# Optimization experiments

Hardware: AMD Instinct MI355X
Metric: run time of the kernel (lower is better)

The kernel has to match this reference:

```python
import jax, jax.numpy as jnp
import numpy as np

N, D, B, P, T = 2048, 64, 64, 16384, 262144
EPS = 1e-6        # const.eps in the original repo
LAST_TIME = 1.0   # init_time = 0


def setup_inputs() -> dict:
    key = jax.random.key(0)
    k = jax.random.split(key, 8)
    x0 = jax.random.normal(k[0], (N, D), dtype=jnp.float32)
    v = 0.1 * jax.random.normal(k[1], (B, N, D), dtype=jnp.float32)
    beta = jax.random.normal(k[2], (N,), dtype=jnp.float32)
    bins_rwidth = jax.random.normal(k[3], (B,), dtype=jnp.float32)
    # distinct node pairs (i != j) to avoid degenerate zero-distance pairs
    i = jax.random.randint(k[4], (P,), 0, N, dtype=jnp.int32)
    off = jax.random.randint(k[5], (P,), 1, N, dtype=jnp.int32)
    node_pairs = jnp.stack([i, (i + off) % N], axis=0)  # [2, P]
    event_times = jax.random.uniform(k[6], (T,), dtype=jnp.float32) * LAST_TIME
    event_pair_idx = jax.random.randint(k[7], (T,), 0, P, dtype=jnp.int32)
    return {"x0": x0, "v": v, "beta": beta, "bins_rwidth": bins_rwidth,
            "event_times": event_times, "node_pairs": node_pairs,
            "event_pair_idx": event_pair_idx}


def reference(x0, v, beta, bins_rwidth, event_times, node_pairs, event_pair_idx):
    # bin bounds: softmax(relative widths) -> cumsum over the timeline
    bounds = jnp.concatenate([jnp.zeros((1,), x0.dtype),
                              jnp.cumsum(jax.nn.softmax(bins_rwidth)) * LAST_TIME])  # [B+1]
    widths = bounds[1:] - bounds[:-1]          # [B]
    inner = bounds[1:-1]                       # bucketize boundaries

    i, j = node_pairs[0], node_pairs[1]
    dx0 = x0[i] - x0[j]                        # [P, D]
    dv = v[:, i, :] - v[:, j, :]               # [B, P, D]
    # cumulative displacement at each bin boundary
    cum = jnp.concatenate([jnp.zeros((1, dx0.shape[0], dx0.shape[1]), dx0.dtype),
                           jnp.cumsum(dv * widths[:, None, None], axis=0)], axis=0)  # [B+1, P, D]
    beta_sum = beta[i] + beta[j]               # [P]

    # ---- intensity integral over the bin bounds (closed form per bin) ----
    idx_b = jnp.searchsorted(inner, bounds, side='right')          # torch.bucketize right=True
    rem_b = bounds - bounds[idx_b]
    xt_b = dx0[None] + cum[idx_b] + dv[idx_b] * rem_b[:, None, None]  # [B+1, P, D]
    norm_b = jnp.linalg.norm(xt_b, axis=2)                         # [B+1, P]
    numer = norm_b * jnp.exp(beta_sum[None, :] - norm_b)
    dot1 = jnp.sum(xt_b[1:] * dv, axis=2)                          # [B, P]
    dot0 = jnp.sum(xt_b[:-1] * dv, axis=2)
    integral = jnp.sum(numer[1:] / (dot1 + EPS) - numer[:-1] / (dot0 + EPS))

    # ---- ragged event log-intensities (flattened: events -> pair ids) ----
    idx_e = jnp.searchsorted(inner, event_times, side='right')     # [T]
    rem_e = event_times - bounds[idx_e]
    pid = event_pair_idx
    xt_e = dx0[pid] + cum[idx_e, pid] + dv[idx_e, pid] * rem_e[:, None]  # [T, D]
    dist_e = jnp.linalg.norm(xt_e, axis=1)
    non_integral = jnp.sum(beta_sum[pid] - dist_e)

    # NLL = -(-integral + non_integral)
    return integral - non_integral
```

## Files before the change

### kernel.cpp

```cpp
#include <hip/hip_runtime.h>

#define NN 2048
#define DD 64
#define BB 64
#define PP 16384
#define TT 262144
#define EPSF 1e-6f
#define SS ((size_t)NN * DD)


typedef unsigned uv2 __attribute__((ext_vector_type(2)));
using bf16x8 = __attribute__((ext_vector_type(8))) short;
using f32x4v = __attribute__((ext_vector_type(4))) float;

template <int CTRL, int RM = 0xF, bool BC = true>
__device__ __forceinline__ float dpp_add(float x) {
    int y = __builtin_amdgcn_update_dpp(0, __float_as_int(x), CTRL, RM, 0xF, BC);
    return x + __int_as_float(y);
}

template <int PAT>
__device__ __forceinline__ float swz_add(float x) {
    return x + __int_as_float(__builtin_amdgcn_ds_swizzle(__float_as_int(x), PAT));
}

__device__ __forceinline__ float xor16_add(float x) {
#if __has_builtin(__builtin_amdgcn_permlane16_swap)
    uv2 r = __builtin_amdgcn_permlane16_swap(__float_as_uint(x), __float_as_uint(x),
                                             false, false);
    return __uint_as_float(r.x) + __uint_as_float(r.y);
#else
    return swz_add<0x401F>(x);
#endif
}
__device__ __forceinline__ float xor32_add(float x) {
#if __has_builtin(__builtin_amdgcn_permlane32_swap)
    uv2 r = __builtin_amdgcn_permlane32_swap(__float_as_uint(x), __float_as_uint(x),
                                             false, false);
    return __uint_as_float(r.x) + __uint_as_float(r.y);
#else
    return x + __shfl_xor(x, 32, 64);
#endif
}

__device__ __forceinline__ float reduce1(float a) {
    a = dpp_add<0xB1>(a);
    a = dpp_add<0x4E>(a);
    a = dpp_add<0x141>(a);
    a = swz_add<0x201F>(a);
    a = xor16_add(a);
    a = xor32_add(a);
    return a;
}

__device__ __forceinline__ float incl_scan(float x) {
    x = dpp_add<0x111>(x);
    x = dpp_add<0x112>(x);
    x = dpp_add<0x114>(x);
    x = dpp_add<0x118>(x);
    x = dpp_add<0x142, 0xA, false>(x);
    x = dpp_add<0x143, 0xC, false>(x);
    return x;
}

__device__ __forceinline__ unsigned short f2bf(float f) {
    unsigned u = __float_as_uint(f);
    unsigned r = (u + 0x7FFFu + ((u >> 16) & 1u)) >> 16;
    return (unsigned short)r;
}
__device__ __forceinline__ float bf_lo(unsigned u) { return __uint_as_float(u << 16); }
__device__ __forceinline__ float bf_hi(unsigned u) { return __uint_as_float(u & 0xFFFF0000u); }

__device__ __forceinline__ unsigned cvt_pk_bf(float lo, float hi) {
    unsigned r;
    asm("v_cvt_pk_bf16_f32 %0, %1, %2" : "=v"(r) : "v"(lo), "v"(hi));
    return r;
}
__device__ __forceinline__ float bpermf(float v, int srclane) {
    return __int_as_float(__builtin_amdgcn_ds_bpermute(srclane << 2, __float_as_int(v)));
}

__global__ void k_bounds(const float* __restrict__ brw, float* __restrict__ bounds,
                         float* __restrict__ widths, float* __restrict__ innerPad,
                         int* __restrict__ cnt, double* __restrict__ acc) {
    if (blockIdx.x != 0) {
        int t = (blockIdx.x - 1) * 64 + threadIdx.x;
#pragma unroll
        for (int k = 0; k < 4; k++) cnt[t * 4 + k] = 0;
        if (blockIdx.x == 1 && threadIdx.x == 0) acc[0] = 0.0;
        return;
    }
    int lane = threadIdx.x;
    float w = brw[lane];
    float m = w;
#pragma unroll
    for (int s = 32; s >= 1; s >>= 1) m = fmaxf(m, __shfl_xor(m, s, 64));
    float e = expf(w - m);
    float tot = e;
#pragma unroll
    for (int s = 32; s >= 1; s >>= 1) tot += __shfl_xor(tot, s, 64);
    float sm = e / tot;
    float c = sm;
#pragma unroll
    for (int off = 1; off < 64; off <<= 1) {
        float t = __shfl_up(c, off, 64);
        if (lane >= off) c += t;
    }
    float cexcl = __shfl_up(c, 1, 64);
    if (lane == 0) cexcl = 0.f;
    if (lane == 0) bounds[0] = 0.f;
    bounds[lane + 1] = c;
    widths[lane] = c - cexcl;
    innerPad[lane] = (lane == 63) ? 3.4e38f : c;
}

__global__ __launch_bounds__(256) void k_convert_hist(const float* __restrict__ v,
                                                      unsigned* __restrict__ vh32,
                                                      const int* __restrict__ pairs,
                                                      int* __restrict__ cnt) {
    if (blockIdx.x >= NN / 4) {
        int t = (blockIdx.x - NN / 4) * 256 + threadIdx.x;
        atomicAdd(&cnt[pairs[t]], 1);
        return;
    }
    int wid = threadIdx.x >> 6, lane = threadIdx.x & 63;
    int n = blockIdx.x * 4 + wid;
    int sub = lane >> 5;
    int dp = (lane & 31) * 2;
    unsigned* __restrict__ dst = vh32 + ((size_t)n * BB * DD) / 2;
#pragma unroll
    for (int c = 0; c < 32; c++) {
        int b = c * 2 + sub;
        float2 f = *(const float2*)(v + (size_t)b * SS + (size_t)n * DD + dp);
        unsigned pk = (unsigned)f2bf(f.x) | ((unsigned)f2bf(f.y) << 16);
        dst[(b * DD + dp) / 2] = pk;
    }
}

__global__ __launch_bounds__(1024) void k_scan2(const int* __restrict__ cnt,
                                                int* __restrict__ cursor) {
    __shared__ int waveTot[16];
    __shared__ int waveOff[16];
    int tid = threadIdx.x;
    int a = cnt[tid * 2], b = cnt[tid * 2 + 1];
    int s = a + b;
    int lane = tid & 63, wid = tid >> 6;
    int incl = s;
#pragma unroll
    for (int off = 1; off < 64; off <<= 1) {
        int t2 = __shfl_up(incl, off, 64);
        if (lane >= off) incl += t2;
    }
    if (lane == 63) waveTot[wid] = incl;
    __syncthreads();
    if (tid == 0) {
        int r = 0;
        for (int w = 0; w < 16; w++) { waveOff[w] = r; r += waveTot[w]; }
    }
    __syncthreads();
    int run = waveOff[wid] + (incl - s);
    cursor[tid * 2] = run;
    cursor[tid * 2 + 1] = run + a;
}

__global__ void k_scatter2(const int* __restrict__ pairs, int* __restrict__ cursor,
                           int* __restrict__ perm) {
    int t = blockIdx.x * 256 + threadIdx.x;
    int pos = atomicAdd(&cursor[pairs[t]], 1);
    perm[pos] = t;
}

__global__ __launch_bounds__(256, 2) void k_pairs(
    const float* __restrict__ x0, const uint4* __restrict__ vh4,
    const float* __restrict__ beta, const int* __restrict__ pairs,
    const int* __restrict__ perm, const float* __restrict__ widths,
    float4* __restrict__ table, double* __restrict__ acc_out) {
    __shared__ double bacc[4];
    const int wid = threadIdx.x >> 6;
    const int lane = threadIdx.x & 63;
    const int bid = blockIdx.x;
    const int vb = ((bid & 7) << 6) | (bid >> 3);
    const int pbase = (vb * 4 + wid) * 8;

    int pk[8], ik[8], jk[8];
    float bs[8];
#pragma unroll
    for (int k = 0; k < 8; k++) pk[k] = perm[pbase + k];
#pragma unroll
    for (int k = 0; k < 8; k++) {
        ik[k] = pairs[pk[k]];
        jk[k] = pairs[PP + pk[k]];
    }
#pragma unroll
    for (int k = 0; k < 8; k++) bs[k] = beta[ik[k]] + beta[jk[k]];

    float wv[4][4];
#pragma unroll
    for (int tm = 0; tm < 4; tm++)
#pragma unroll
        for (int r = 0; r < 4; r++)
            wv[tm][r] = widths[16 * tm + (lane >> 4) * 4 + r];
    const float wl = widths[lane];
    const int laneterm = (lane & 15) * 8 + (lane >> 4);
    const int nl = lane & 15;
    const int mb = (lane >> 4) * 4;

    uint4 ra0[8], rb0[8], ra1[8], rb1[8];
    float xi0, xj0, xi1, xj1;

#define ISSUE(RA, RB, XI, XJ, k_)                                            \
    {                                                                        \
        const uint4* Vi = vh4 + (size_t)ik[k_] * 512 + laneterm;             \
        const uint4* Vj = vh4 + (size_t)jk[k_] * 512 + laneterm;             \
        _Pragma("unroll") for (int t = 0; t < 4; t++) {                      \
            RA[t * 2 + 0] = Vi[t * 128];                                     \
            RA[t * 2 + 1] = Vi[t * 128 + 4];                                 \
            RB[t * 2 + 0] = Vj[t * 128];                                     \
            RB[t * 2 + 1] = Vj[t * 128 + 4];                                 \
        }                                                                    \
        XI = x0[ik[k_] * DD + lane];                                         \
        XJ = x0[jk[k_] * DD + lane];                                         \
    }

    double accd = 0.0;

#define STEP(RA, RB, XI, XJ, k_, NEXTISSUE)                                                    \
    {                                                                                          \
        const float bsum = bs[k_];                                                             \
        float dx0 = XI - XJ;                                                                   \
        float n2_0 = reduce1(dx0 * dx0);                                                       \
        float rr0 = __builtin_amdgcn_sqrtf(n2_0);                                              \
        float numer0 = rr0 * __expf(bsum - rr0);                                               \
        bf16x8 F[8];                                                                           \
        _Pragma("unroll") for (int f = 0; f < 8; f++) {                                        \
            uint4 q;                                                                           \
            q.x = cvt_pk_bf(bf_lo(RA[f].x) - bf_lo(RB[f].x), bf_hi(RA[f].x) - bf_hi(RB[f].x)); \
            q.y = cvt_pk_bf(bf_lo(RA[f].y) - bf_lo(RB[f].y), bf_hi(RA[f].y) - bf_hi(RB[f].y)); \
            q.z = cvt_pk_bf(bf_lo(RA[f].z) - bf_lo(RB[f].z), bf_hi(RA[f].z) - bf_hi(RB[f].z)); \
            q.w = cvt_pk_bf(bf_lo(RA[f].w) - bf_lo(RB[f].w), bf_hi(RA[f].w) - bf_hi(RB[f].w)); \
            union { uint4 u; bf16x8 s; } cv;                                                   \
            cv.u = q;                                                                          \
            F[f] = cv.s;                                                                       \
        }                                                                                      \
        NEXTISSUE                                                                              \
        bf16x8 AX[2];                                                                          \
        _Pragma("unroll") for (int kb = 0; kb < 2; kb++) {                                     \
            unsigned u[4];                                                                     \
            _Pragma("unroll") for (int c2 = 0; c2 < 4; c2++) {                                 \
                int k0 = kb * 32 + ((lane >> 4) << 3) + c2 * 2;                                \
                u[c2] = cvt_pk_bf(bpermf(dx0, k0), bpermf(dx0, k0 + 1));                       \
            }                                                                                  \
            uint4 q;                                                                           \
            bool z = (lane & 15) != 0;                                                         \
            q.x = z ? 0u : u[0]; q.y = z ? 0u : u[1];                                          \
            q.z = z ? 0u : u[2]; q.w = z ? 0u : u[3];                                          \
            union { uint4 uu; bf16x8 s; } cv;                                                  \
            cv.uu = q;                                                                         \
            AX[kb] = cv.s;                                                                     \
        }                                                                                      \
        f32x4v g00 = {0.f, 0.f, 0.f, 0.f}, g01 = g00, g02 = g00, g03 = g00;                    \
        f32x4v g11 = g00, g12 = g00, g13 = g00, g22 = g00, g23 = g00, g33 = g00;               \
        GMM(g00, 0, 0) GMM(g01, 0, 1) GMM(g02, 0, 2) GMM(g03, 0, 3)                            \
        GMM(g11, 1, 1) GMM(g12, 1, 2) GMM(g13, 1, 3)                                           \
        GMM(g22, 2, 2) GMM(g23, 2, 3) GMM(g33, 3, 3)                                           \
        float c00, c01, c02, c03;                                                              \
        {                                                                                      \
            f32x4v ca = {0.f, 0.f, 0.f, 0.f};                                                  \
            CMM(0) c00 = ca[0]; ca = {0.f, 0.f, 0.f, 0.f};                                     \
            CMM(1) c01 = ca[0]; ca = {0.f, 0.f, 0.f, 0.f};                                     \
            CMM(2) c02 = ca[0]; ca = {0.f, 0.f, 0.f, 0.f};                                     \
            CMM(3) c03 = ca[0];                                                                \
        }                                                                                      \
        float c0v;                                                                             \
        {                                                                                      \
            float b0 = bpermf(c00, lane & 15);                                                 \
            float b1 = bpermf(c01, lane & 15);                                                 \
            float b2 = bpermf(c02, lane & 15);                                                 \
            float b3 = bpermf(c03, lane & 15);                                                 \
            int g = lane >> 4;                                                                 \
            c0v = (g == 0) ? b0 : (g == 1) ? b1 : (g == 2) ? b2 : b3;                          \
        }                                                                                      \
        float Sv = 0.f, qv = 0.f;                                                              \
        { float sp = 0.f, qp = 0.f;                                 DIAG(g00, 0) FINTN(0) }    \
        { float sp = OFFT(g01, 0), qp = 0.f;                        DIAG(g11, 1) FINTN(1) }    \
        { float sp = OFFT(g02, 0) + OFFT(g12, 1), qp = 0.f;         DIAG(g22, 2) FINTN(2) }    \
        { float sp = OFFT(g03, 0) + OFFT(g13, 1) + OFFT(g23, 2), qp = 0.f;                     \
                                                                    DIAG(g33, 3) FINTN(3) }    \
        float d0r = c0v + Sv;                                                                  \
        float qqr = qv;                                                                        \
        float tt = wl * fmaf(wl, qqr, 2.f * d0r);                                              \
        float incl = incl_scan(tt);                                                            \
        float n2L = fmaxf(n2_0 + (incl - tt), 0.f);                                            \
        float n2R = fmaxf(n2_0 + incl, 0.f);                                                   \
        float rrR = __builtin_amdgcn_sqrtf(n2R);                                               \
        float numerR = rrR * __expf(bsum - rrR);                                               \
        float numerL = __int_as_float(                                                         \
            __builtin_amdgcn_update_dpp(0, __float_as_int(numerR), 0x138, 0xF, 0xF, true));    \
        numerL = (lane == 0) ? numer0 : numerL;                                                \
        float pd = fmaf(wl, qqr, d0r);                                                         \
        float term = numerR * __builtin_amdgcn_rcpf(pd + EPSF)                                 \
                   - numerL * __builtin_amdgcn_rcpf(d0r + EPSF);                               \
        float acc = reduce1(term);                                                             \
        table[(size_t)pk[k_] * BB + lane] = make_float4(n2L, d0r, qqr, bsum);                  \
        accd += (double)acc;                                                                   \
    }

#define GMM(acc, ta, tb)                                                                       \
    acc = __builtin_amdgcn_mfma_f32_16x16x32_bf16(F[(ta)*2 + 0], F[(tb)*2 + 0], acc, 0, 0, 0); \
    acc = __builtin_amdgcn_mfma_f32_16x16x32_bf16(F[(ta)*2 + 1], F[(tb)*2 + 1], acc, 0, 0, 0);
#define CMM(tb)                                                                       \
    ca = __builtin_amdgcn_mfma_f32_16x16x32_bf16(AX[0], F[(tb)*2 + 0], ca, 0, 0, 0); \
    ca = __builtin_amdgcn_mfma_f32_16x16x32_bf16(AX[1], F[(tb)*2 + 1], ca, 0, 0, 0);
#define OFFT(gt, t_) (wv[t_][0] * gt[0] + wv[t_][1] * gt[1] + wv[t_][2] * gt[2] + wv[t_][3] * gt[3])
#define DIAG(d, t_)                                       \
    sp += (mb + 0 < nl) ? wv[t_][0] * d[0] : 0.f;         \
    sp += (mb + 1 < nl) ? wv[t_][1] * d[1] : 0.f;         \
    sp += (mb + 2 < nl) ? wv[t_][2] * d[2] : 0.f;         \
    sp += (mb + 3 < nl) ? wv[t_][3] * d[3] : 0.f;         \
    qp += (mb + 0 == nl) ? d[0] : 0.f;                    \
    qp += (mb + 1 == nl) ? d[1] : 0.f;                    \
    qp += (mb + 2 == nl) ? d[2] : 0.f;                    \
    qp += (mb + 3 == nl) ? d[3] : 0.f;
#define FINTN(t_)                                         \
    sp = xor16_add(sp); sp = xor32_add(sp);               \
    qp = xor16_add(qp); qp = xor32_add(qp);               \
    if ((lane >> 4) == t_) { Sv = sp; qv = qp; }

    ISSUE(ra0, rb0, xi0, xj0, 0)
    ISSUE(ra1, rb1, xi1, xj1, 1)

    STEP(ra0, rb0, xi0, xj0, 0, ISSUE(ra0, rb0, xi0, xj0, 2))
    STEP(ra1, rb1, xi1, xj1, 1, ISSUE(ra1, rb1, xi1, xj1, 3))
    STEP(ra0, rb0, xi0, xj0, 2, ISSUE(ra0, rb0, xi0, xj0, 4))
    STEP(ra1, rb1, xi1, xj1, 3, ISSUE(ra1, rb1, xi1, xj1, 5))
    STEP(ra0, rb0, xi0, xj0, 4, ISSUE(ra0, rb0, xi0, xj0, 6))
    STEP(ra1, rb1, xi1, xj1, 5, ISSUE(ra1, rb1, xi1, xj1, 7))
    STEP(ra0, rb0, xi0, xj0, 6, )
    STEP(ra1, rb1, xi1, xj1, 7, )

#undef ISSUE
#undef STEP
#undef GMM
#undef CMM
#undef OFFT
#undef DIAG
#undef FINTN

    if (lane == 0) bacc[wid] = accd;
    __syncthreads();
    if (threadIdx.x == 0)
        atomicAdd(acc_out, bacc[0] + bacc[1] + bacc[2] + bacc[3]);
}

__global__ __launch_bounds__(256) void k_events(
    const float* __restrict__ times, const int* __restrict__ epid,
    const float* __restrict__ bounds, const float* __restrict__ innerPad,
    const float4* __restrict__ table, double* __restrict__ acc_out) {
    __shared__ float si[64];
    __shared__ float sb[BB + 1];
    __shared__ double wacc[4];
    int tid = threadIdx.x;
    if (tid < 64) si[tid] = innerPad[tid];
    if (tid <= BB) sb[tid] = bounds[tid];
    __syncthreads();
    int g = (blockIdx.x * 256 + tid) * 2;
    float2 tm2 = *(const float2*)(times + g);
    int2 pd2 = *(const int2*)(epid + g);
    float tms[2] = {tm2.x, tm2.y};
    int pids[2] = {pd2.x, pd2.y};
    int cc[2];
    float rem[2];
#pragma unroll
    for (int k = 0; k < 2; k++) {
        int c = 0;
        float tm = tms[k];
#pragma unroll
        for (int s = 32; s >= 1; s >>= 1)
            if (si[c + s - 1] <= tm) c += s;
        cc[k] = c;
        rem[k] = tm - sb[c];
    }
    float4 e0 = table[(size_t)pids[0] * BB + cc[0]];
    float4 e1 = table[(size_t)pids[1] * BB + cc[1]];
    float eacc;
    {
        float d2 = fmaxf(fmaf(rem[0], fmaf(rem[0], e0.z, 2.f * e0.y), e0.x), 0.f);
        eacc = e0.w - __builtin_amdgcn_sqrtf(d2);
        d2 = fmaxf(fmaf(rem[1], fmaf(rem[1], e1.z, 2.f * e1.y), e1.x), 0.f);
        eacc += e1.w - __builtin_amdgcn_sqrtf(d2);
    }
    float val = reduce1(eacc);
    if ((tid & 63) == 0) wacc[tid >> 6] = (double)val;
    __syncthreads();
    if (tid == 0)
        atomicAdd(acc_out, -(wacc[0] + wacc[1] + wacc[2] + wacc[3]));
}

__global__ void k_finalize(const double* __restrict__ acc, float* __restrict__ out) {
    out[0] = (float)(*acc);
}

extern "C" void kernel_launch(void* const* d_in, const int* in_sizes, int n_in,
                              void* d_out, int out_size, void* d_ws, size_t ws_size,
                              hipStream_t stream) {
    const float* x0     = (const float*)d_in[0];
    const float* v      = (const float*)d_in[1];
    const float* beta   = (const float*)d_in[2];
    const float* brw    = (const float*)d_in[3];
    const float* etimes = (const float*)d_in[4];
    const int*   pairs  = (const int*)d_in[5];
    const int*   epid   = (const int*)d_in[6];

    char* ws = (char*)d_ws;
    double* acc     = (double*)ws;
    int* cnt        = (int*)(ws + 1024);
    int* cursor     = (int*)(ws + 9216);
    int* perm       = (int*)(ws + 17408);
    float* bounds   = (float*)(ws + 82944);
    float* widths   = (float*)(ws + 83456);
    float* innerPad = (float*)(ws + 83968);
    float4* table   = (float4*)(ws + 84480);
    unsigned* vh32  = (unsigned*)(ws + 84480 + (size_t)PP * BB * 16);

    hipLaunchKernelGGL(k_bounds, dim3(9), dim3(64), 0, stream, brw, bounds, widths,
                       innerPad, cnt, acc);
    hipLaunchKernelGGL(k_convert_hist, dim3(NN / 4 + PP / 256), dim3(256), 0, stream,
                       v, vh32, pairs, cnt);
    hipLaunchKernelGGL(k_scan2, dim3(1), dim3(1024), 0, stream, cnt, cursor);
    hipLaunchKernelGGL(k_scatter2, dim3(PP / 256), dim3(256), 0, stream, pairs, cursor, perm);
    hipLaunchKernelGGL(k_pairs, dim3(PP / 32), dim3(256), 0, stream, x0, (const uint4*)vh32,
                       beta, pairs, perm, widths, table, acc);
    hipLaunchKernelGGL(k_events, dim3(TT / 512), dim3(256), 0, stream, etimes, epid,
                       bounds, innerPad, table, acc);
    hipLaunchKernelGGL(k_finalize, dim3(1), dim3(1), 0, stream, acc, (float*)d_out);
}
```

Measured before the change: 76.86 us.

## Fuse preprocessing kernels into one launch and finalize via last-block counter

Merges bounds computation, the v-to-bf16 conversion, the pair histogram, the scan and the scatter into a single kernel, k_pre. The histogram, scan and permutation now run in one block using shared-memory atomics. The conversion and the table writes use nontemporal vector loads and stores, and the MFMA section is raised with s_setprio. The separate finalize kernel is replaced by a last-block-done counter in k_events. Together these remove four launches and the global-memory round trips for counts and cursors, at the cost of serialising all the permutation work in one block.

```diff
diff --git a/kernel.cpp b/kernel.cpp
--- a/kernel.cpp
+++ b/kernel.cpp
@@ -10,6 +10,8 @@
 
 
 typedef unsigned uv2 __attribute__((ext_vector_type(2)));
+typedef float fx4 __attribute__((ext_vector_type(4)));
+typedef unsigned ux4 __attribute__((ext_vector_type(4)));
 using bf16x8 = __attribute__((ext_vector_type(8))) short;
 using f32x4v = __attribute__((ext_vector_type(4))) float;
 
@@ -63,10 +65,9 @@
     return x;
 }
 
-__device__ __forceinline__ unsigned short f2bf(float f) {
+__device__ __forceinline__ unsigned f2bf(float f) {
     unsigned u = __float_as_uint(f);
-    unsigned r = (u + 0x7FFFu + ((u >> 16) & 1u)) >> 16;
-    return (unsigned short)r;
+    return (u + 0x7FFFu + ((u >> 16) & 1u)) >> 16;
 }
 __device__ __forceinline__ float bf_lo(unsigned u) { return __uint_as_float(u << 16); }
 __device__ __forceinline__ float bf_hi(unsigned u) { return __uint_as_float(u & 0xFFFF0000u); }
@@ -80,70 +81,73 @@
     return __int_as_float(__builtin_amdgcn_ds_bpermute(srclane << 2, __float_as_int(v)));
 }
 
-__global__ void k_bounds(const float* __restrict__ brw, float* __restrict__ bounds,
-                         float* __restrict__ widths, float* __restrict__ innerPad,
-                         int* __restrict__ cnt, double* __restrict__ acc) {
-    if (blockIdx.x != 0) {
-        int t = (blockIdx.x - 1) * 64 + threadIdx.x;
-#pragma unroll
-        for (int k = 0; k < 4; k++) cnt[t * 4 + k] = 0;
-        if (blockIdx.x == 1 && threadIdx.x == 0) acc[0] = 0.0;
-        return;
-    }
-    int lane = threadIdx.x;
-    float w = brw[lane];
-    float m = w;
-#pragma unroll
-    for (int s = 32; s >= 1; s >>= 1) m = fmaxf(m, __shfl_xor(m, s, 64));
-    float e = expf(w - m);
-    float tot = e;
-#pragma unroll
-    for (int s = 32; s >= 1; s >>= 1) tot += __shfl_xor(tot, s, 64);
-    float sm = e / tot;
-    float c = sm;
-#pragma unroll
-    for (int off = 1; off < 64; off <<= 1) {
-        float t = __shfl_up(c, off, 64);
-        if (lane >= off) c += t;
-    }
-    float cexcl = __shfl_up(c, 1, 64);
-    if (lane == 0) cexcl = 0.f;
-    if (lane == 0) bounds[0] = 0.f;
-    bounds[lane + 1] = c;
-    widths[lane] = c - cexcl;
-    innerPad[lane] = (lane == 63) ? 3.4e38f : c;
-}
-
-__global__ __launch_bounds__(256) void k_convert_hist(const float* __restrict__ v,
-                                                      unsigned* __restrict__ vh32,
-                                                      const int* __restrict__ pairs,
-                                                      int* __restrict__ cnt) {
-    if (blockIdx.x >= NN / 4) {
-        int t = (blockIdx.x - NN / 4) * 256 + threadIdx.x;
-        atomicAdd(&cnt[pairs[t]], 1);
-        return;
-    }
-    int wid = threadIdx.x >> 6, lane = threadIdx.x & 63;
-    int n = blockIdx.x * 4 + wid;
-    int sub = lane >> 5;
-    int dp = (lane & 31) * 2;
-    unsigned* __restrict__ dst = vh32 + ((size_t)n * BB * DD) / 2;
-#pragma unroll
-    for (int c = 0; c < 32; c++) {
-        int b = c * 2 + sub;
-        float2 f = *(const float2*)(v + (size_t)b * SS + (size_t)n * DD + dp);
-        unsigned pk = (unsigned)f2bf(f.x) | ((unsigned)f2bf(f.y) << 16);
-        dst[(b * DD + dp) / 2] = pk;
-    }
-}
-
-__global__ __launch_bounds__(1024) void k_scan2(const int* __restrict__ cnt,
-                                                int* __restrict__ cursor) {
+__global__ __launch_bounds__(1024) void k_pre(
+    const float* __restrict__ v, unsigned* __restrict__ vh32,
+    const float* __restrict__ brw, float* __restrict__ bounds,
+    float* __restrict__ widths, float* __restrict__ innerPad,
+    const int* __restrict__ pairs, int* __restrict__ perm,
+    double* __restrict__ acc, int* __restrict__ done) {
+    __shared__ int scnt[2048];
     __shared__ int waveTot[16];
     __shared__ int waveOff[16];
-    int tid = threadIdx.x;
-    int a = cnt[tid * 2], b = cnt[tid * 2 + 1];
-    int s = a + b;
+    const int bid = blockIdx.x;
+    const int tid = threadIdx.x;
+
+    if (bid < 1024) {
+        const int bin = bid >> 4;
+        const int node0 = (bid & 15) << 7;
+        const fx4* __restrict__ src =
+            (const fx4*)(v + (size_t)bin * SS + (size_t)node0 * DD);
+        fx4 f0 = __builtin_nontemporal_load(src + tid * 2);
+        fx4 f1 = __builtin_nontemporal_load(src + tid * 2 + 1);
+        const int nn = tid >> 3;
+        const int d = (tid & 7) * 8;
+        ux4 o;
+        o.x = f2bf(f0.x) | (f2bf(f0.y) << 16);
+        o.y = f2bf(f0.z) | (f2bf(f0.w) << 16);
+        o.z = f2bf(f1.x) | (f2bf(f1.y) << 16);
+        o.w = f2bf(f1.z) | (f2bf(f1.w) << 16);
+        *(ux4*)(vh32 + (size_t)(node0 + nn) * 2048 + bin * 32 + d / 2) = o;
+        return;
+    }
+
+    if (bid == 1024) {
+        if (tid == 64) *acc = 0.0;
+        if (tid == 65) *done = 0;
+        if (tid >= 64) return;
+        int lane = tid;
+        float w = brw[lane];
+        float m = w;
+#pragma unroll
+        for (int s = 32; s >= 1; s >>= 1) m = fmaxf(m, __shfl_xor(m, s, 64));
+        float e = expf(w - m);
+        float tot = e;
+#pragma unroll
+        for (int s = 32; s >= 1; s >>= 1) tot += __shfl_xor(tot, s, 64);
+        float sm = e / tot;
+        float c = sm;
+#pragma unroll
+        for (int off = 1; off < 64; off <<= 1) {
+            float t = __shfl_up(c, off, 64);
+            if (lane >= off) c += t;
+        }
+        float cexcl = __shfl_up(c, 1, 64);
+        if (lane == 0) cexcl = 0.f;
+        if (lane == 0) bounds[0] = 0.f;
+        bounds[lane + 1] = c;
+        widths[lane] = c - cexcl;
+        innerPad[lane] = (lane == 63) ? 3.4e38f : c;
+        return;
+    }
+
+    scnt[tid] = 0;
+    scnt[tid + 1024] = 0;
+    __syncthreads();
+#pragma unroll
+    for (int k = 0; k < 16; k++) atomicAdd(&scnt[pairs[k * 1024 + tid]], 1);
+    __syncthreads();
+    int a = scnt[tid * 2], b2 = scnt[tid * 2 + 1];
+    int s = a + b2;
     int lane = tid & 63, wid = tid >> 6;
     int incl = s;
 #pragma unroll
@@ -159,22 +163,22 @@
     }
     __syncthreads();
     int run = waveOff[wid] + (incl - s);
-    cursor[tid * 2] = run;
-    cursor[tid * 2 + 1] = run + a;
-}
-
-__global__ void k_scatter2(const int* __restrict__ pairs, int* __restrict__ cursor,
-                           int* __restrict__ perm) {
-    int t = blockIdx.x * 256 + threadIdx.x;
-    int pos = atomicAdd(&cursor[pairs[t]], 1);
-    perm[pos] = t;
+    scnt[tid * 2] = run;
+    scnt[tid * 2 + 1] = run + a;
+    __syncthreads();
+#pragma unroll
+    for (int k = 0; k < 16; k++) {
+        int idx = k * 1024 + tid;
+        int pos = atomicAdd(&scnt[pairs[idx]], 1);
+        perm[pos] = idx;
+    }
 }
 
 __global__ __launch_bounds__(256, 2) void k_pairs(
     const float* __restrict__ x0, const uint4* __restrict__ vh4,
     const float* __restrict__ beta, const int* __restrict__ pairs,
     const int* __restrict__ perm, const float* __restrict__ widths,
-    float4* __restrict__ table, double* __restrict__ acc_out) {
+    float* __restrict__ table, double* __restrict__ acc_out) {
     __shared__ double bacc[4];
     const int wid = threadIdx.x >> 6;
     const int lane = threadIdx.x & 63;
@@ -258,6 +262,7 @@
             cv.uu = q;                                                                         \
             AX[kb] = cv.s;                                                                     \
         }                                                                                      \
+        __builtin_amdgcn_s_setprio(1);                                                         \
         f32x4v g00 = {0.f, 0.f, 0.f, 0.f}, g01 = g00, g02 = g00, g03 = g00;                    \
         f32x4v g11 = g00, g12 = g00, g13 = g00, g22 = g00, g23 = g00, g33 = g00;               \
         GMM(g00, 0, 0) GMM(g01, 0, 1) GMM(g02, 0, 2) GMM(g03, 0, 3)                            \
@@ -271,6 +276,7 @@
             CMM(2) c02 = ca[0]; ca = {0.f, 0.f, 0.f, 0.f};                                     \
             CMM(3) c03 = ca[0];                                                                \
         }                                                                                      \
+        __builtin_amdgcn_s_setprio(0);                                                         \
         float c0v;                                                                             \
         {                                                                                      \
             float b0 = bpermf(c00, lane & 15);                                                 \
@@ -301,7 +307,10 @@
         float term = numerR * __builtin_amdgcn_rcpf(pd + EPSF)                                 \
                    - numerL * __builtin_amdgcn_rcpf(d0r + EPSF);                               \
         float acc = reduce1(term);                                                             \
-        table[(size_t)pk[k_] * BB + lane] = make_float4(n2L, d0r, qqr, bsum);                  \
+        fx4 outv;                                                                              \
+        outv.x = n2L; outv.y = d0r; outv.z = qqr; outv.w = bsum;                               \
+        __builtin_nontemporal_store(outv,                                                      \
+            (fx4*)(table + ((size_t)pk[k_] * BB + lane) * 4));                                 \
         accd += (double)acc;                                                                   \
     }
 
@@ -355,7 +364,8 @@
 __global__ __launch_bounds__(256) void k_events(
     const float* __restrict__ times, const int* __restrict__ epid,
     const float* __restrict__ bounds, const float* __restrict__ innerPad,
-    const float4* __restrict__ table, double* __restrict__ acc_out) {
+    const float4* __restrict__ table, double* __restrict__ acc_out,
+    int* __restrict__ done, float* __restrict__ out) {
     __shared__ float si[64];
     __shared__ float sb[BB + 1];
     __shared__ double wacc[4];
@@ -392,12 +402,15 @@
     float val = reduce1(eacc);
     if ((tid & 63) == 0) wacc[tid >> 6] = (double)val;
     __syncthreads();
-    if (tid == 0)
+    if (tid == 0) {
         atomicAdd(acc_out, -(wacc[0] + wacc[1] + wacc[2] + wacc[3]));
-}
-
-__global__ void k_finalize(const double* __restrict__ acc, float* __restrict__ out) {
-    out[0] = (float)(*acc);
+        __threadfence();
+        int c = atomicAdd(done, 1);
+        if (c == (int)gridDim.x - 1) {
+            double a = atomicAdd(acc_out, 0.0);
+            out[0] = (float)a;
+        }
+    }
 }
 
 extern "C" void kernel_launch(void* const* d_in, const int* in_sizes, int n_in,
@@ -413,24 +426,18 @@
 
     char* ws = (char*)d_ws;
     double* acc     = (double*)ws;
-    int* cnt        = (int*)(ws + 1024);
-    int* cursor     = (int*)(ws + 9216);
+    int* done       = (int*)(ws + 1024);
     int* perm       = (int*)(ws + 17408);
     float* bounds   = (float*)(ws + 82944);
     float* widths   = (float*)(ws + 83456);
     float* innerPad = (float*)(ws + 83968);
-    float4* table   = (float4*)(ws + 84480);
+    float* table    = (float*)(ws + 84480);
     unsigned* vh32  = (unsigned*)(ws + 84480 + (size_t)PP * BB * 16);
 
-    hipLaunchKernelGGL(k_bounds, dim3(9), dim3(64), 0, stream, brw, bounds, widths,
-                       innerPad, cnt, acc);
-    hipLaunchKernelGGL(k_convert_hist, dim3(NN / 4 + PP / 256), dim3(256), 0, stream,
-                       v, vh32, pairs, cnt);
-    hipLaunchKernelGGL(k_scan2, dim3(1), dim3(1024), 0, stream, cnt, cursor);
-    hipLaunchKernelGGL(k_scatter2, dim3(PP / 256), dim3(256), 0, stream, pairs, cursor, perm);
+    hipLaunchKernelGGL(k_pre, dim3(1026), dim3(1024), 0, stream, v, vh32, brw,
+                       bounds, widths, innerPad, pairs, perm, acc, done);
     hipLaunchKernelGGL(k_pairs, dim3(PP / 32), dim3(256), 0, stream, x0, (const uint4*)vh32,
                        beta, pairs, perm, widths, table, acc);
     hipLaunchKernelGGL(k_events, dim3(TT / 512), dim3(256), 0, stream, etimes, epid,
-                       bounds, innerPad, table, acc);
-    hipLaunchKernelGGL(k_finalize, dim3(1), dim3(1), 0, stream, acc, (float*)d_out);
-}
+                       bounds, innerPad, (const float4*)table, acc, done, (float*)d_out);
+}
```

Measured after the change: 93.67 us. +21.9%, slower.
